# Performance work log

Measured on AMD Instinct MI355X. Metric: run time of the kernel, lower is better.

## Reference

```python
import jax, jax.numpy as jnp
import numpy as np

B, S, H, D = 2, 2048, 2048, 256  # batch, seq, hidden, head_dim
NH, NKV = 8, 1                   # attention heads, kv heads
N_REP = NH // NKV
SCALING = D ** -0.5
ROPE_THETA = 10000.0
NEG_INF = -1e9


def rotate_half(x):
    x1, x2 = jnp.split(x, 2, axis=-1)
    return jnp.concatenate((-x2, x1), axis=-1)


def setup_inputs() -> dict:
    key = jax.random.key(0)
    ks = jax.random.split(key, 5)
    hidden_states = jax.random.normal(ks[0], (B, S, H), dtype=jnp.float32)
    # RoPE cos/sin per position, Gemma-style: inv_freq tiled over full head_dim
    inv_freq = 1.0 / (ROPE_THETA ** (np.arange(0, D, 2, dtype=np.float32) / D))  # [D/2]
    pos = np.arange(S, dtype=np.float32)
    freqs = np.outer(pos, inv_freq)                      # [S, D/2]
    emb = np.concatenate([freqs, freqs], axis=-1)        # [S, D]
    cos = jnp.broadcast_to(jnp.asarray(np.cos(emb)), (B, S, D))
    sin = jnp.broadcast_to(jnp.asarray(np.sin(emb)), (B, S, D))
    # additive causal mask [B, 1, S, S]
    causal = jnp.triu(jnp.full((S, S), NEG_INF, dtype=jnp.float32), k=1)
    attention_mask = jnp.broadcast_to(causal[None, None], (B, 1, S, S))
    scale = 0.02
    Wq = jax.random.normal(ks[1], (H, NH * D), dtype=jnp.float32) * scale
    Wk = jax.random.normal(ks[2], (H, NKV * D), dtype=jnp.float32) * scale
    Wv = jax.random.normal(ks[3], (H, NKV * D), dtype=jnp.float32) * scale
    Wo = jax.random.normal(ks[4], (NH * D, H), dtype=jnp.float32) * scale
    return {"hidden_states": hidden_states, "cos": cos, "sin": sin,
            "attention_mask": attention_mask, "Wq": Wq, "Wk": Wk, "Wv": Wv, "Wo": Wo}


def reference(hidden_states, cos, sin, attention_mask, Wq, Wk, Wv, Wo):
    # projections: [B,S,H] @ [H, nh*D] -> [B, nh, S, D]
    q = (hidden_states @ Wq).reshape(B, S, NH, D).transpose(0, 2, 1, 3)
    k = (hidden_states @ Wk).reshape(B, S, NKV, D).transpose(0, 2, 1, 3)
    v = (hidden_states @ Wv).reshape(B, S, NKV, D).transpose(0, 2, 1, 3)
    # RoPE (cos/sin broadcast over head dim via unsqueeze at axis 1)
    c = cos[:, None]  # [B,1,S,D]
    s = sin[:, None]
    q = q * c + rotate_half(q) * s
    k = k * c + rotate_half(k) * s
    # repeat_kv: [B, NKV, S, D] -> [B, NH, S, D]
    k = jnp.repeat(k, N_REP, axis=1)
    v = jnp.repeat(v, N_REP, axis=1)
    # eager attention
    attn_weights = jnp.einsum("bhqd,bhkd->bhqk", q, k) * SCALING
    attn_weights = attn_weights + attention_mask[:, :, :, :S]
    attn_weights = jax.nn.softmax(attn_weights.astype(jnp.float32), axis=-1).astype(q.dtype)
    attn_output = jnp.einsum("bhqk,bhkd->bhqd", attn_weights, v)
    attn_output = attn_output.transpose(0, 2, 1, 3).reshape(B, S, NH * D)
    attn_output = attn_output @ Wo
    return attn_output, attn_weights
```

## Files before the change

kernel.cpp:

```cpp
#include <hip/hip_runtime.h>
#include <hip/hip_bf16.h>

#define B_   2
#define S_   2048
#define H_   2048
#define D_   256
#define NH_  8

typedef unsigned short u16;
typedef __bf16 bf16x8 __attribute__((ext_vector_type(8)));
typedef float f32x4 __attribute__((ext_vector_type(4)));
typedef unsigned int uint4v __attribute__((ext_vector_type(4)));
typedef unsigned int uint2v __attribute__((ext_vector_type(2)));

__device__ __forceinline__ u16 f2bf(float x) {
  union { float f; unsigned u; } v; v.f = x;
  unsigned u = v.u;
  u += 0x7FFFu + ((u >> 16) & 1u);
  return (u16)(u >> 16);
}
__device__ __forceinline__ float bf2f(u16 x) {
  union { unsigned u; float f; } v; v.u = ((unsigned)x) << 16;
  return v.f;
}

#define BM 128
#define BN 128
#define BK 32
#define LDSS 40

enum GemmMode { MODE_PROJ = 0, MODE_QK = 1, MODE_PV = 2, MODE_WO = 3 };

template <int MODE>
__global__ __launch_bounds__(256)
void gemm_nt(const void* __restrict__ Ap, const u16* __restrict__ Bp,
             void* __restrict__ Cp, int K, int lda, int ldb, int ldc)
{
  const int bn = blockIdx.x, bm = blockIdx.y, bz = blockIdx.z;
  if (MODE == MODE_QK && bn > bm) return;

  const int m0 = bm * BM, n0 = bn * BN;

  const u16*   A16 = (const u16*)Ap;
  const float* A32 = (const float*)Ap;
  const u16*   Bb  = Bp;
  float* Cf = (float*)Cp;
  u16*   Cu = (u16*)Cp;

  if constexpr (MODE == MODE_QK) {
    A16 += (size_t)bz * S_ * D_;
    Bb  += (size_t)(bz >> 3) * S_ * D_;
    Cf  += (size_t)bz * S_ * S_;
  } else if constexpr (MODE == MODE_PV) {
    A32 += (size_t)bz * S_ * S_;
    Bb  += (size_t)(bz >> 3) * D_ * S_;
    Cu  += (size_t)(bz >> 3) * S_ * (NH_ * D_) + (size_t)(bz & 7) * D_;
  }

  int Keff = K;
  if constexpr (MODE == MODE_PV) {
    int lim = (bm + 1) * BM;
    Keff = lim < K ? lim : K;
  }

  __shared__ __align__(16) u16 As[BM * LDSS];
  __shared__ __align__(16) u16 Bs[BN * LDSS];

  const int tid  = threadIdx.x;
  const int lane = tid & 63;
  const int wave = tid >> 6;
  const int quad = lane >> 4;
  const int l16  = lane & 15;
  const int wm   = (wave >> 1) << 6;
  const int wn   = (wave & 1) << 6;

  const f32x4 zero4 = {0.f, 0.f, 0.f, 0.f};
  f32x4 acc[4][4];
  #pragma unroll
  for (int i = 0; i < 4; i++)
    #pragma unroll
    for (int j = 0; j < 4; j++)
      acc[i][j] = zero4;

  for (int kt = 0; kt < Keff; kt += BK) {
    if constexpr (MODE == MODE_PV) {
      #pragma unroll
      for (int i = 0; i < 4; i++) {
        int c   = tid + i * 256;
        int row = c >> 3, kc = c & 7;
        const float4 f = *(const float4*)(A32 + (size_t)(m0 + row) * lda + kt + kc * 4);
        uint2v p;
        p.x = (unsigned)f2bf(f.x) | ((unsigned)f2bf(f.y) << 16);
        p.y = (unsigned)f2bf(f.z) | ((unsigned)f2bf(f.w) << 16);
        *(uint2v*)(&As[row * LDSS + kc * 4]) = p;
      }
    } else {
      #pragma unroll
      for (int i = 0; i < 2; i++) {
        int c   = tid + i * 256;
        int row = c >> 2, kc = c & 3;
        *(uint4v*)(&As[row * LDSS + kc * 8]) =
            *(const uint4v*)(A16 + (size_t)(m0 + row) * lda + kt + kc * 8);
      }
    }
    #pragma unroll
    for (int i = 0; i < 2; i++) {
      int c   = tid + i * 256;
      int row = c >> 2, kc = c & 3;
      *(uint4v*)(&Bs[row * LDSS + kc * 8]) =
          *(const uint4v*)(Bb + (size_t)(n0 + row) * ldb + kt + kc * 8);
    }
    __syncthreads();

    bf16x8 af[4], bfr[4];
    #pragma unroll
    for (int i = 0; i < 4; i++)
      af[i] = *(const bf16x8*)(&As[(wm + i * 16 + l16) * LDSS + quad * 8]);
    #pragma unroll
    for (int j = 0; j < 4; j++)
      bfr[j] = *(const bf16x8*)(&Bs[(wn + j * 16 + l16) * LDSS + quad * 8]);
    #pragma unroll
    for (int i = 0; i < 4; i++)
      #pragma unroll
      for (int j = 0; j < 4; j++)
        acc[i][j] = __builtin_amdgcn_mfma_f32_16x16x32_bf16(af[i], bfr[j], acc[i][j], 0, 0, 0);
    __syncthreads();
  }

  #pragma unroll
  for (int i = 0; i < 4; i++) {
    #pragma unroll
    for (int j = 0; j < 4; j++) {
      #pragma unroll
      for (int r = 0; r < 4; r++) {
        int m = m0 + wm + i * 16 + quad * 4 + r;
        int n = n0 + wn + j * 16 + l16;
        float v = acc[i][j][r];
        if constexpr (MODE == MODE_QK) {
          v *= 0.0625f;
          if (n > m) v += -1.0e9f;
          Cf[(size_t)m * ldc + n] = v;
        } else if constexpr (MODE == MODE_WO) {
          Cf[(size_t)m * ldc + n] = v;
        } else {
          Cu[(size_t)m * ldc + n] = f2bf(v);
        }
      }
    }
  }
}

__global__ __launch_bounds__(256)
void convert_bf16_kernel(const float* __restrict__ src, u16* __restrict__ dst, int n4)
{
  int i = blockIdx.x * 256 + threadIdx.x;
  if (i >= n4) return;
  float4 f = ((const float4*)src)[i];
  uint2v p;
  p.x = (unsigned)f2bf(f.x) | ((unsigned)f2bf(f.y) << 16);
  p.y = (unsigned)f2bf(f.z) | ((unsigned)f2bf(f.w) << 16);
  ((uint2v*)dst)[i] = p;
}

__global__ __launch_bounds__(256)
void transpose_convert(const float* __restrict__ src, u16* __restrict__ dst, int K, int N)
{
  __shared__ float t[32][33];
  int n0 = blockIdx.x * 32, k0 = blockIdx.y * 32;
  int c = threadIdx.x & 31, r = threadIdx.x >> 5;
  #pragma unroll
  for (int rr = 0; rr < 32; rr += 8)
    t[r + rr][c] = src[(size_t)(k0 + r + rr) * N + n0 + c];
  __syncthreads();
  #pragma unroll
  for (int rr = 0; rr < 32; rr += 8)
    dst[(size_t)(n0 + r + rr) * K + k0 + c] = f2bf(t[c][r + rr]);
}

__global__ __launch_bounds__(256)
void transpose_v_kernel(const u16* __restrict__ v, u16* __restrict__ vt)
{
  __shared__ u16 t[32][34];
  int b = blockIdx.z;
  int d0 = blockIdx.x * 32, s0 = blockIdx.y * 32;
  int c = threadIdx.x & 31, r = threadIdx.x >> 5;
  #pragma unroll
  for (int rr = 0; rr < 32; rr += 8)
    t[r + rr][c] = v[(size_t)b * S_ * D_ + (size_t)(s0 + r + rr) * D_ + d0 + c];
  __syncthreads();
  #pragma unroll
  for (int rr = 0; rr < 32; rr += 8)
    vt[(size_t)b * D_ * S_ + (size_t)(d0 + r + rr) * S_ + s0 + c] = t[c][r + rr];
}

__global__ __launch_bounds__(256)
void rope_q_kernel(const u16* __restrict__ qraw, const float* __restrict__ cosb,
                   const float* __restrict__ sinb, u16* __restrict__ qout)
{
  int idx = blockIdx.x;
  int h = idx & 7, bs = idx >> 3;
  int b = bs >> 11, s = bs & (S_ - 1);
  int d = threadIdx.x;
  size_t base = (size_t)bs * (NH_ * D_) + (size_t)h * D_;
  float qv = bf2f(qraw[base + d]);
  float qp = bf2f(qraw[base + (d ^ 128)]);
  float c  = cosb[(size_t)bs * D_ + d];
  float sn = sinb[(size_t)bs * D_ + d];
  float rot = (d < 128) ? -qp : qp;
  qout[(((size_t)b * NH_ + h) * S_ + s) * D_ + d] = f2bf(qv * c + rot * sn);
}

__global__ __launch_bounds__(256)
void rope_k_kernel(const u16* __restrict__ kraw, const float* __restrict__ cosb,
                   const float* __restrict__ sinb, u16* __restrict__ kout)
{
  int bs = blockIdx.x;
  int d = threadIdx.x;
  size_t base = (size_t)bs * D_;
  float kv = bf2f(kraw[base + d]);
  float kp = bf2f(kraw[base + (d ^ 128)]);
  float c  = cosb[(size_t)bs * D_ + d];
  float sn = sinb[(size_t)bs * D_ + d];
  float rot = (d < 128) ? -kp : kp;
  kout[base + d] = f2bf(kv * c + rot * sn);
}

__global__ __launch_bounds__(256)
void softmax_rows(float* __restrict__ attn)
{
  const int r = blockIdx.x;
  const int q = r & (S_ - 1);
  float* row = attn + (size_t)r * S_;
  const int t = threadIdx.x;
  const int lane = t & 63, wave = t >> 6;

  float vals[8];
  float mx = -3.0e38f;
  #pragma unroll
  for (int i = 0; i < 8; i++) {
    int k = i * 256 + t;
    float v = (k <= q) ? row[k] : -3.0e38f;
    vals[i] = v;
    mx = fmaxf(mx, v);
  }
  #pragma unroll
  for (int o = 32; o >= 1; o >>= 1) mx = fmaxf(mx, __shfl_xor(mx, o, 64));
  __shared__ float redm[4];
  if (lane == 0) redm[wave] = mx;
  __syncthreads();
  mx = fmaxf(fmaxf(redm[0], redm[1]), fmaxf(redm[2], redm[3]));

  float sum = 0.f;
  #pragma unroll
  for (int i = 0; i < 8; i++) {
    int k = i * 256 + t;
    float e = (k <= q) ? expf(vals[i] - mx) : 0.f;
    vals[i] = e;
    sum += e;
  }
  #pragma unroll
  for (int o = 32; o >= 1; o >>= 1) sum += __shfl_xor(sum, o, 64);
  __shared__ float reds[4];
  if (lane == 0) reds[wave] = sum;
  __syncthreads();
  sum = reds[0] + reds[1] + reds[2] + reds[3];

  float inv = 1.0f / sum;
  #pragma unroll
  for (int i = 0; i < 8; i++)
    row[i * 256 + t] = vals[i] * inv;
}

extern "C" void kernel_launch(void* const* d_in, const int* in_sizes, int n_in,
                              void* d_out, int out_size, void* d_ws, size_t ws_size,
                              hipStream_t stream)
{
  const float* X    = (const float*)d_in[0];
  const float* cosb = (const float*)d_in[1];
  const float* sinb = (const float*)d_in[2];
  const float* Wq   = (const float*)d_in[4];
  const float* Wk   = (const float*)d_in[5];
  const float* Wv   = (const float*)d_in[6];
  const float* Wo   = (const float*)d_in[7];

  float* outO = (float*)d_out;
  float* outP = outO + (size_t)B_ * S_ * H_;

  u16* ws   = (u16*)d_ws;
  u16* Xbf  = ws;
  u16* WqT  = Xbf  + 8388608;
  u16* WkT  = WqT  + 4194304;
  u16* WvT  = WkT  + 524288;
  u16* WoT  = WvT  + 524288;
  u16* Qraw = WoT  + 4194304;
  u16* Kraw = Qraw + 8388608;
  u16* Vraw = Kraw + 1048576;
  u16* Qbf  = Xbf;
  u16* Kbf  = WqT;
  u16* VT   = WqT + 1048576;
  u16* AObf = Qraw;

  convert_bf16_kernel<<<8192, 256, 0, stream>>>(X, Xbf, 2097152);
  transpose_convert<<<dim3(64, 64), 256, 0, stream>>>(Wq, WqT, 2048, 2048);
  transpose_convert<<<dim3(8, 64),  256, 0, stream>>>(Wk, WkT, 2048, 256);
  transpose_convert<<<dim3(8, 64),  256, 0, stream>>>(Wv, WvT, 2048, 256);
  transpose_convert<<<dim3(64, 64), 256, 0, stream>>>(Wo, WoT, 2048, 2048);
  gemm_nt<MODE_PROJ><<<dim3(16, 32, 1), 256, 0, stream>>>(Xbf, WqT, Qraw, 2048, 2048, 2048, 2048);
  gemm_nt<MODE_PROJ><<<dim3(2, 32, 1),  256, 0, stream>>>(Xbf, WkT, Kraw, 2048, 2048, 2048, 256);
  gemm_nt<MODE_PROJ><<<dim3(2, 32, 1),  256, 0, stream>>>(Xbf, WvT, Vraw, 2048, 2048, 2048, 256);
  rope_q_kernel<<<32768, 256, 0, stream>>>(Qraw, cosb, sinb, Qbf);
  rope_k_kernel<<<4096, 256, 0, stream>>>(Kraw, cosb, sinb, Kbf);
  transpose_v_kernel<<<dim3(8, 64, 2), 256, 0, stream>>>(Vraw, VT);
  gemm_nt<MODE_QK><<<dim3(16, 16, 16), 256, 0, stream>>>(Qbf, Kbf, outP, 256, 256, 256, 2048);
  softmax_rows<<<32768, 256, 0, stream>>>(outP);
  gemm_nt<MODE_PV><<<dim3(2, 16, 16), 256, 0, stream>>>(outP, VT, AObf, 2048, 2048, 2048, 2048);
  gemm_nt<MODE_WO><<<dim3(16, 32, 1), 256, 0, stream>>>(AObf, WoT, outO, 2048, 2048, 2048, 2048);
}
```

Baseline: 787.0 us.

## Fuse QKV GEMM, fold softmax exp into QK epilogue, use direct global-to-LDS loads

QKV projections become one GEMM into a packed buffer. The QK GEMM epilogue now computes unnormalized exp2 scores without a max-subtraction, stores them as bf16 and atomically accumulates row sums. A light normalize kernel writes the fp32 probabilities, and the PV GEMM reads the bf16 exp values and divides by the row sum in its epilogue. GEMM tiles load through global_load_lds without LDS padding. This removes the fp32 score round trip and the separate softmax pass, but skipping max-subtraction risks overflow for large logits, and the unpadded LDS layout may add bank conflicts.

```diff
diff --git a/kernel.cpp b/kernel.cpp
--- a/kernel.cpp
+++ b/kernel.cpp
@@ -13,6 +13,9 @@
 typedef unsigned int uint4v __attribute__((ext_vector_type(4)));
 typedef unsigned int uint2v __attribute__((ext_vector_type(2)));
 
+#define AS1 __attribute__((address_space(1)))
+#define AS3 __attribute__((address_space(3)))
+
 __device__ __forceinline__ u16 f2bf(float x) {
   union { float f; unsigned u; } v; v.f = x;
   unsigned u = v.u;
@@ -24,37 +27,42 @@
   return v.f;
 }
 
+__device__ __forceinline__ void gld_lds16(const u16* g, u16* l) {
+  __builtin_amdgcn_global_load_lds((const AS1 unsigned int*)g,
+                                   (AS3 unsigned int*)l, 16, 0, 0);
+}
+
 #define BM 128
 #define BN 128
 #define BK 32
-#define LDSS 40
 
 enum GemmMode { MODE_PROJ = 0, MODE_QK = 1, MODE_PV = 2, MODE_WO = 3 };
 
 template <int MODE>
 __global__ __launch_bounds__(256)
-void gemm_nt(const void* __restrict__ Ap, const u16* __restrict__ Bp,
-             void* __restrict__ Cp, int K, int lda, int ldb, int ldc)
+void gemm_nt(const u16* __restrict__ A, const u16* __restrict__ Bb,
+             void* __restrict__ Cp, float* __restrict__ rows,
+             int K, int lda, int ldb, int ldc)
 {
   const int bn = blockIdx.x, bm = blockIdx.y, bz = blockIdx.z;
   if (MODE == MODE_QK && bn > bm) return;
-
   const int m0 = bm * BM, n0 = bn * BN;
 
-  const u16*   A16 = (const u16*)Ap;
-  const float* A32 = (const float*)Ap;
-  const u16*   Bb  = Bp;
+  const u16* Ap = A;
+  const u16* Bp = Bb;
   float* Cf = (float*)Cp;
   u16*   Cu = (u16*)Cp;
 
   if constexpr (MODE == MODE_QK) {
-    A16 += (size_t)bz * S_ * D_;
-    Bb  += (size_t)(bz >> 3) * S_ * D_;
-    Cf  += (size_t)bz * S_ * S_;
+    Ap   += (size_t)bz * S_ * D_;
+    Bp   += (size_t)(bz >> 3) * S_ * D_;
+    Cu   += (size_t)bz * S_ * S_;
+    rows += (size_t)bz * S_;
   } else if constexpr (MODE == MODE_PV) {
-    A32 += (size_t)bz * S_ * S_;
-    Bb  += (size_t)(bz >> 3) * D_ * S_;
-    Cu  += (size_t)(bz >> 3) * S_ * (NH_ * D_) + (size_t)(bz & 7) * D_;
+    Ap   += (size_t)bz * S_ * S_;
+    Bp   += (size_t)(bz >> 3) * D_ * S_;
+    Cu   += (size_t)(bz >> 3) * S_ * (NH_ * D_) + (size_t)(bz & 7) * D_;
+    rows += (size_t)bz * S_;
   }
 
   int Keff = K;
@@ -63,62 +71,39 @@
     Keff = lim < K ? lim : K;
   }
 
-  __shared__ __align__(16) u16 As[BM * LDSS];
-  __shared__ __align__(16) u16 Bs[BN * LDSS];
+  __shared__ __align__(16) u16 As[BM * BK];
+  __shared__ __align__(16) u16 Bs[BN * BK];
 
   const int tid  = threadIdx.x;
   const int lane = tid & 63;
-  const int wave = tid >> 6;
   const int quad = lane >> 4;
   const int l16  = lane & 15;
+  const int wave = tid >> 6;
   const int wm   = (wave >> 1) << 6;
   const int wn   = (wave & 1) << 6;
 
-  const f32x4 zero4 = {0.f, 0.f, 0.f, 0.f};
-  f32x4 acc[4][4];
-  #pragma unroll
-  for (int i = 0; i < 4; i++)
-    #pragma unroll
-    for (int j = 0; j < 4; j++)
-      acc[i][j] = zero4;
+  f32x4 acc[4][4] = {};
 
   for (int kt = 0; kt < Keff; kt += BK) {
-    if constexpr (MODE == MODE_PV) {
-      #pragma unroll
-      for (int i = 0; i < 4; i++) {
-        int c   = tid + i * 256;
-        int row = c >> 3, kc = c & 7;
-        const float4 f = *(const float4*)(A32 + (size_t)(m0 + row) * lda + kt + kc * 4);
-        uint2v p;
-        p.x = (unsigned)f2bf(f.x) | ((unsigned)f2bf(f.y) << 16);
-        p.y = (unsigned)f2bf(f.z) | ((unsigned)f2bf(f.w) << 16);
-        *(uint2v*)(&As[row * LDSS + kc * 4]) = p;
-      }
-    } else {
-      #pragma unroll
-      for (int i = 0; i < 2; i++) {
-        int c   = tid + i * 256;
-        int row = c >> 2, kc = c & 3;
-        *(uint4v*)(&As[row * LDSS + kc * 8]) =
-            *(const uint4v*)(A16 + (size_t)(m0 + row) * lda + kt + kc * 8);
-      }
+    #pragma unroll
+    for (int i = 0; i < 2; i++) {
+      int c = tid + i * 256;
+      gld_lds16(Ap + (size_t)(m0 + (c >> 2)) * lda + kt + (c & 3) * 8, &As[c * 8]);
     }
     #pragma unroll
     for (int i = 0; i < 2; i++) {
-      int c   = tid + i * 256;
-      int row = c >> 2, kc = c & 3;
-      *(uint4v*)(&Bs[row * LDSS + kc * 8]) =
-          *(const uint4v*)(Bb + (size_t)(n0 + row) * ldb + kt + kc * 8);
+      int c = tid + i * 256;
+      gld_lds16(Bp + (size_t)(n0 + (c >> 2)) * ldb + kt + (c & 3) * 8, &Bs[c * 8]);
     }
     __syncthreads();
 
     bf16x8 af[4], bfr[4];
     #pragma unroll
     for (int i = 0; i < 4; i++)
-      af[i] = *(const bf16x8*)(&As[(wm + i * 16 + l16) * LDSS + quad * 8]);
+      af[i] = *(const bf16x8*)(&As[(wm + i * 16 + l16) * BK + quad * 8]);
     #pragma unroll
     for (int j = 0; j < 4; j++)
-      bfr[j] = *(const bf16x8*)(&Bs[(wn + j * 16 + l16) * LDSS + quad * 8]);
+      bfr[j] = *(const bf16x8*)(&Bs[(wn + j * 16 + l16) * BK + quad * 8]);
     #pragma unroll
     for (int i = 0; i < 4; i++)
       #pragma unroll
@@ -127,23 +112,42 @@
     __syncthreads();
   }
 
+  const float SCL2 = 0.0625f * 1.44269504088896340736f;
   #pragma unroll
   for (int i = 0; i < 4; i++) {
     #pragma unroll
-    for (int j = 0; j < 4; j++) {
-      #pragma unroll
-      for (int r = 0; r < 4; r++) {
-        int m = m0 + wm + i * 16 + quad * 4 + r;
-        int n = n0 + wn + j * 16 + l16;
-        float v = acc[i][j][r];
-        if constexpr (MODE == MODE_QK) {
-          v *= 0.0625f;
-          if (n > m) v += -1.0e9f;
-          Cf[(size_t)m * ldc + n] = v;
-        } else if constexpr (MODE == MODE_WO) {
-          Cf[(size_t)m * ldc + n] = v;
-        } else {
-          Cu[(size_t)m * ldc + n] = f2bf(v);
+    for (int r = 0; r < 4; r++) {
+      const int m = m0 + wm + i * 16 + quad * 4 + r;
+      if constexpr (MODE == MODE_QK) {
+        float rs = 0.f;
+        #pragma unroll
+        for (int j = 0; j < 4; j++) {
+          int n = n0 + wn + j * 16 + l16;
+          float e = (n <= m) ? exp2f(acc[i][j][r] * SCL2) : 0.f;
+          rs += e;
+          Cu[(size_t)m * ldc + n] = f2bf(e);
+        }
+        #pragma unroll
+        for (int o = 1; o < 16; o <<= 1) rs += __shfl_xor(rs, o, 64);
+        if (l16 == 0) atomicAdd(&rows[m], rs);
+      } else if constexpr (MODE == MODE_PV) {
+        float inv = 1.0f / rows[m];
+        #pragma unroll
+        for (int j = 0; j < 4; j++) {
+          int n = n0 + wn + j * 16 + l16;
+          Cu[(size_t)m * ldc + n] = f2bf(acc[i][j][r] * inv);
+        }
+      } else if constexpr (MODE == MODE_WO) {
+        #pragma unroll
+        for (int j = 0; j < 4; j++) {
+          int n = n0 + wn + j * 16 + l16;
+          Cf[(size_t)m * ldc + n] = acc[i][j][r];
+        }
+      } else {
+        #pragma unroll
+        for (int j = 0; j < 4; j++) {
+          int n = n0 + wn + j * 16 + l16;
+          Cu[(size_t)m * ldc + n] = f2bf(acc[i][j][r]);
         }
       }
     }
@@ -186,7 +190,7 @@
   int c = threadIdx.x & 31, r = threadIdx.x >> 5;
   #pragma unroll
   for (int rr = 0; rr < 32; rr += 8)
-    t[r + rr][c] = v[(size_t)b * S_ * D_ + (size_t)(s0 + r + rr) * D_ + d0 + c];
+    t[r + rr][c] = v[(size_t)(b * S_ + s0 + r + rr) * 2560 + 2304 + d0 + c];
   __syncthreads();
   #pragma unroll
   for (int rr = 0; rr < 32; rr += 8)
@@ -201,7 +205,7 @@
   int h = idx & 7, bs = idx >> 3;
   int b = bs >> 11, s = bs & (S_ - 1);
   int d = threadIdx.x;
-  size_t base = (size_t)bs * (NH_ * D_) + (size_t)h * D_;
+  size_t base = (size_t)bs * 2560 + (size_t)h * D_;
   float qv = bf2f(qraw[base + d]);
   float qp = bf2f(qraw[base + (d ^ 128)]);
   float c  = cosb[(size_t)bs * D_ + d];
@@ -216,59 +220,45 @@
 {
   int bs = blockIdx.x;
   int d = threadIdx.x;
-  size_t base = (size_t)bs * D_;
+  size_t base = (size_t)bs * 2560 + 2048;
   float kv = bf2f(kraw[base + d]);
   float kp = bf2f(kraw[base + (d ^ 128)]);
   float c  = cosb[(size_t)bs * D_ + d];
   float sn = sinb[(size_t)bs * D_ + d];
   float rot = (d < 128) ? -kp : kp;
-  kout[base + d] = f2bf(kv * c + rot * sn);
-}
-
-__global__ __launch_bounds__(256)
-void softmax_rows(float* __restrict__ attn)
+  kout[(size_t)bs * D_ + d] = f2bf(kv * c + rot * sn);
+}
+
+__global__ __launch_bounds__(256)
+void normalize_p(const u16* __restrict__ E, const float* __restrict__ rows,
+                 float* __restrict__ P)
 {
   const int r = blockIdx.x;
   const int q = r & (S_ - 1);
-  float* row = attn + (size_t)r * S_;
-  const int t = threadIdx.x;
-  const int lane = t & 63, wave = t >> 6;
-
-  float vals[8];
-  float mx = -3.0e38f;
-  #pragma unroll
-  for (int i = 0; i < 8; i++) {
-    int k = i * 256 + t;
-    float v = (k <= q) ? row[k] : -3.0e38f;
-    vals[i] = v;
-    mx = fmaxf(mx, v);
-  }
-  #pragma unroll
-  for (int o = 32; o >= 1; o >>= 1) mx = fmaxf(mx, __shfl_xor(mx, o, 64));
-  __shared__ float redm[4];
-  if (lane == 0) redm[wave] = mx;
-  __syncthreads();
-  mx = fmaxf(fmaxf(redm[0], redm[1]), fmaxf(redm[2], redm[3]));
-
-  float sum = 0.f;
-  #pragma unroll
-  for (int i = 0; i < 8; i++) {
-    int k = i * 256 + t;
-    float e = (k <= q) ? expf(vals[i] - mx) : 0.f;
-    vals[i] = e;
-    sum += e;
-  }
-  #pragma unroll
-  for (int o = 32; o >= 1; o >>= 1) sum += __shfl_xor(sum, o, 64);
-  __shared__ float reds[4];
-  if (lane == 0) reds[wave] = sum;
-  __syncthreads();
-  sum = reds[0] + reds[1] + reds[2] + reds[3];
-
-  float inv = 1.0f / sum;
-  #pragma unroll
-  for (int i = 0; i < 8; i++)
-    row[i * 256 + t] = vals[i] * inv;
+  const u16* e = E + (size_t)r * S_;
+  float* p = P + (size_t)r * S_;
+  const float inv = 1.0f / rows[r];
+  const int k0 = threadIdx.x * 8;
+
+  float4 lo = {0.f, 0.f, 0.f, 0.f}, hi = {0.f, 0.f, 0.f, 0.f};
+  if (k0 <= q) {
+    uint4v u = *(const uint4v*)(e + k0);
+    float v[8];
+    v[0] = bf2f(u.x & 0xffff); v[1] = bf2f(u.x >> 16);
+    v[2] = bf2f(u.y & 0xffff); v[3] = bf2f(u.y >> 16);
+    v[4] = bf2f(u.z & 0xffff); v[5] = bf2f(u.z >> 16);
+    v[6] = bf2f(u.w & 0xffff); v[7] = bf2f(u.w >> 16);
+    lo.x = (k0 + 0 <= q) ? v[0] * inv : 0.f;
+    lo.y = (k0 + 1 <= q) ? v[1] * inv : 0.f;
+    lo.z = (k0 + 2 <= q) ? v[2] * inv : 0.f;
+    lo.w = (k0 + 3 <= q) ? v[3] * inv : 0.f;
+    hi.x = (k0 + 4 <= q) ? v[4] * inv : 0.f;
+    hi.y = (k0 + 5 <= q) ? v[5] * inv : 0.f;
+    hi.z = (k0 + 6 <= q) ? v[6] * inv : 0.f;
+    hi.w = (k0 + 7 <= q) ? v[7] * inv : 0.f;
+  }
+  *(float4*)(p + k0)     = lo;
+  *(float4*)(p + k0 + 4) = hi;
 }
 
 extern "C" void kernel_launch(void* const* d_in, const int* in_sizes, int n_in,
@@ -286,33 +276,34 @@
   float* outO = (float*)d_out;
   float* outP = outO + (size_t)B_ * S_ * H_;
 
-  u16* ws   = (u16*)d_ws;
-  u16* Xbf  = ws;
-  u16* WqT  = Xbf  + 8388608;
-  u16* WkT  = WqT  + 4194304;
-  u16* WvT  = WkT  + 524288;
-  u16* WoT  = WvT  + 524288;
-  u16* Qraw = WoT  + 4194304;
-  u16* Kraw = Qraw + 8388608;
-  u16* Vraw = Kraw + 1048576;
-  u16* Qbf  = Xbf;
-  u16* Kbf  = WqT;
-  u16* VT   = WqT + 1048576;
-  u16* AObf = Qraw;
+  u16* ws     = (u16*)d_ws;
+  u16* Xbf    = ws;
+  u16* WT     = Xbf    + 8388608;
+  u16* WoT    = WT     + 5242880;
+  u16* QKVraw = WoT    + 4194304;
+  u16* Qbf    = QKVraw + 10485760;
+  u16* Kbf    = Qbf    + 8388608;
+  u16* VT     = Kbf    + 1048576;
+  u16* AObf   = VT     + 1048576;
+  u16* Ebf    = AObf   + 8388608;
+  float* Rows = (float*)(Ebf + 67108864);
 
   convert_bf16_kernel<<<8192, 256, 0, stream>>>(X, Xbf, 2097152);
-  transpose_convert<<<dim3(64, 64), 256, 0, stream>>>(Wq, WqT, 2048, 2048);
-  transpose_convert<<<dim3(8, 64),  256, 0, stream>>>(Wk, WkT, 2048, 256);
-  transpose_convert<<<dim3(8, 64),  256, 0, stream>>>(Wv, WvT, 2048, 256);
+  transpose_convert<<<dim3(64, 64), 256, 0, stream>>>(Wq, WT, 2048, 2048);
+  transpose_convert<<<dim3(8, 64),  256, 0, stream>>>(Wk, WT + 2048 * 2048, 2048, 256);
+  transpose_convert<<<dim3(8, 64),  256, 0, stream>>>(Wv, WT + 2304 * 2048, 2048, 256);
   transpose_convert<<<dim3(64, 64), 256, 0, stream>>>(Wo, WoT, 2048, 2048);
-  gemm_nt<MODE_PROJ><<<dim3(16, 32, 1), 256, 0, stream>>>(Xbf, WqT, Qraw, 2048, 2048, 2048, 2048);
-  gemm_nt<MODE_PROJ><<<dim3(2, 32, 1),  256, 0, stream>>>(Xbf, WkT, Kraw, 2048, 2048, 2048, 256);
-  gemm_nt<MODE_PROJ><<<dim3(2, 32, 1),  256, 0, stream>>>(Xbf, WvT, Vraw, 2048, 2048, 2048, 256);
-  rope_q_kernel<<<32768, 256, 0, stream>>>(Qraw, cosb, sinb, Qbf);
-  rope_k_kernel<<<4096, 256, 0, stream>>>(Kraw, cosb, sinb, Kbf);
-  transpose_v_kernel<<<dim3(8, 64, 2), 256, 0, stream>>>(Vraw, VT);
-  gemm_nt<MODE_QK><<<dim3(16, 16, 16), 256, 0, stream>>>(Qbf, Kbf, outP, 256, 256, 256, 2048);
-  softmax_rows<<<32768, 256, 0, stream>>>(outP);
-  gemm_nt<MODE_PV><<<dim3(2, 16, 16), 256, 0, stream>>>(outP, VT, AObf, 2048, 2048, 2048, 2048);
-  gemm_nt<MODE_WO><<<dim3(16, 32, 1), 256, 0, stream>>>(AObf, WoT, outO, 2048, 2048, 2048, 2048);
-}
+  gemm_nt<MODE_PROJ><<<dim3(20, 32, 1), 256, 0, stream>>>(
+      Xbf, WT, QKVraw, nullptr, 2048, 2048, 2048, 2560);
+  rope_q_kernel<<<32768, 256, 0, stream>>>(QKVraw, cosb, sinb, Qbf);
+  rope_k_kernel<<<4096, 256, 0, stream>>>(QKVraw, cosb, sinb, Kbf);
+  transpose_v_kernel<<<dim3(8, 64, 2), 256, 0, stream>>>(QKVraw, VT);
+  hipMemsetAsync(Rows, 0, 32768 * sizeof(float), stream);
+  gemm_nt<MODE_QK><<<dim3(16, 16, 16), 256, 0, stream>>>(
+      Qbf, Kbf, Ebf, Rows, 256, 256, 256, 2048);
+  normalize_p<<<32768, 256, 0, stream>>>(Ebf, Rows, outP);
+  gemm_nt<MODE_PV><<<dim3(2, 16, 16), 256, 0, stream>>>(
+      Ebf, VT, AObf, Rows, 2048, 2048, 2048, 2048);
+  gemm_nt<MODE_WO><<<dim3(16, 32, 1), 256, 0, stream>>>(
+      AObf, WoT, outO, nullptr, 2048, 2048, 2048, 2048);
+}
```

New measurement: 706.4 us. -10.2%, faster.
